# Kernel optimization log

Measured on AMD Instinct MI355X. Metric: run time of the kernel, lower is better.

Reference implementation:

```python
import jax, jax.numpy as jnp
import numpy as np

T, R, HEADS, H, L = 4, 8, 4, 128, 2
DK = H // HEADS
NPT = 25000
N = T * NPT
E = 600000
IN_DIMS = [512, 256, 128, 64]


def setup_inputs() -> dict:
    key = jax.random.key(0)
    ks = iter(jax.random.split(key, 64))
    d = {}
    # per-type raw node features (concatenation order = type order)
    for i, di in enumerate(IN_DIMS):
        d[f"nf{i}"] = jax.random.normal(next(ks), (NPT, di), jnp.float32)
    # per-type input encoder MLPs: Linear(di,256) -> ReLU -> Linear(256,H)
    for i, di in enumerate(IN_DIMS):
        d[f"enc_w1_{i}"] = jax.random.normal(next(ks), (di, 256), jnp.float32) * (1.0 / np.sqrt(di))
        d[f"enc_b1_{i}"] = jnp.zeros((256,), jnp.float32)
        d[f"enc_w2_{i}"] = jax.random.normal(next(ks), (256, H), jnp.float32) * (1.0 / np.sqrt(256))
        d[f"enc_b2_{i}"] = jnp.zeros((H,), jnp.float32)
    # HGT conv params, stacked over L layers
    sc = 1.0 / np.sqrt(H)
    for nm in ["Wk", "Wq", "Wv", "Wa"]:
        d[nm] = jax.random.normal(next(ks), (L, T, H, H), jnp.float32) * sc
        d["b" + nm[1]] = jnp.zeros((L, T, H), jnp.float32)
    eye = jnp.broadcast_to(jnp.eye(DK, dtype=jnp.float32), (L, R, HEADS, DK, DK))
    d["rel_att"] = eye + 0.05 * jax.random.normal(next(ks), (L, R, HEADS, DK, DK), jnp.float32)
    d["rel_msg"] = eye + 0.05 * jax.random.normal(next(ks), (L, R, HEADS, DK, DK), jnp.float32)
    d["rel_pri"] = jnp.ones((L, R, HEADS), jnp.float32)
    d["skip"] = jnp.zeros((L, T), jnp.float32)  # sigmoid(0)=0.5 gate
    d["gamma"] = jnp.ones((L, H), jnp.float32)
    d["beta"] = jnp.zeros((L, H), jnp.float32)
    # graph structure
    d["node_types"] = jnp.repeat(jnp.arange(T, dtype=jnp.int32), NPT)
    d["edge_index"] = jax.random.randint(next(ks), (2, E), 0, N, jnp.int32)
    d["edge_types"] = jax.random.randint(next(ks), (E,), 0, R, jnp.int32)
    return d


def typed_linear(x, nt, W, b):
    # W: [T,H,H], b: [T,H]; select per-node-type transform
    allt = jnp.einsum('nd,tdh->tnh', x, W) + b[:, None, :]  # [T,N,H]
    return allt[nt, jnp.arange(x.shape[0])]  # [N,H]


def layer_norm(x, g, b):
    m = x.mean(-1, keepdims=True)
    v = jnp.var(x, -1, keepdims=True)
    return (x - m) * jax.lax.rsqrt(v + 1e-5) * g + b


def hgt_layer(h, nt, src, dst, et, Wk, bk, Wq, bq, Wv, bv, Wa, ba, ra, rm, rp, skip, g, be):
    n = h.shape[0]
    k = typed_linear(h, nt, Wk, bk).reshape(n, HEADS, DK)
    q = typed_linear(h, nt, Wq, bq).reshape(n, HEADS, DK)
    v = typed_linear(h, nt, Wv, bv).reshape(n, HEADS, DK)
    k_s, v_s, q_d = k[src], v[src], q[dst]  # [E,HEADS,DK]
    # relation-conditioned key/message transforms (small fixed loop over R relations)
    kt = jnp.zeros_like(k_s)
    mt = jnp.zeros_like(v_s)
    for r in range(R):
        msk = (et == r)[:, None, None]
        kt = kt + jnp.where(msk, jnp.einsum('ehd,hdf->ehf', k_s, ra[r]), 0.0)
        mt = mt + jnp.where(msk, jnp.einsum('ehd,hdf->ehf', v_s, rm[r]), 0.0)
    att = (q_d * kt).sum(-1) * rp[et] * (1.0 / np.sqrt(DK))  # [E,HEADS]
    # segment softmax over incoming edges of each target node
    amax = jax.ops.segment_max(att, dst, num_segments=n)
    amax = jnp.where(jnp.isfinite(amax), amax, 0.0)
    ea = jnp.exp(att - amax[dst])
    den = jax.ops.segment_sum(ea, dst, num_segments=n)
    w = ea / jnp.maximum(den[dst], 1e-9)
    res = jax.ops.segment_sum(w[:, :, None] * mt, dst, num_segments=n).reshape(n, H)
    trans = typed_linear(jax.nn.gelu(res, approximate=False), nt, Wa, ba)
    alpha = jax.nn.sigmoid(skip)[nt][:, None]
    out = trans * alpha + h * (1.0 - alpha)
    return layer_norm(out, g, be)


def reference(nf0, nf1, nf2, nf3,
              enc_w1_0, enc_b1_0, enc_w2_0, enc_b2_0,
              enc_w1_1, enc_b1_1, enc_w2_1, enc_b2_1,
              enc_w1_2, enc_b1_2, enc_w2_2, enc_b2_2,
              enc_w1_3, enc_b1_3, enc_w2_3, enc_b2_3,
              Wk, bk, Wq, bq, Wv, bv, Wa, ba,
              rel_att, rel_msg, rel_pri, skip, gamma, beta,
              node_types, edge_index, edge_types):
    encs = [(enc_w1_0, enc_b1_0, enc_w2_0, enc_b2_0),
            (enc_w1_1, enc_b1_1, enc_w2_1, enc_b2_1),
            (enc_w1_2, enc_b1_2, enc_w2_2, enc_b2_2),
            (enc_w1_3, enc_b1_3, enc_w2_3, enc_b2_3)]
    embs = [jax.nn.relu(nf @ w1 + b1) @ w2 + b2
            for nf, (w1, b1, w2, b2) in zip([nf0, nf1, nf2, nf3], encs)]
    h = jnp.concatenate(embs, axis=0)  # [N,H]; dropout is identity in eval mode
    src, dst = edge_index[0], edge_index[1]
    for l in range(L):
        h = hgt_layer(h, node_types, src, dst, edge_types,
                      Wk[l], bk[l], Wq[l], bq[l], Wv[l], bv[l], Wa[l], ba[l],
                      rel_att[l], rel_msg[l], rel_pri[l], skip[l], gamma[l], beta[l])
    return h
```

## Files before the change

kernel.cpp:

```cpp
#include <hip/hip_runtime.h>
#include <math.h>


#define NPT   25000
#define NN    100000
#define EE    600000
#define HD    128
#define NRELS 8

typedef unsigned short u16;
typedef unsigned int   u32;
using s16x8 = __attribute__((ext_vector_type(8))) short;
using f32x4 = __attribute__((ext_vector_type(4))) float;

__device__ __forceinline__ u16 f2bf(float x){
  u32 u = __float_as_uint(x);
  u += 0x7fffu + ((u >> 16) & 1u);
  return (u16)(u >> 16);
}
__device__ __forceinline__ float bf2f(u16 v){ return __uint_as_float(((u32)v) << 16); }

__global__ __launch_bounds__(256) void cast_tr(const float* __restrict__ in,
                                               u16* __restrict__ out, int K, int N){
  long b = blockIdx.y;
  const float* ib = in + b * (long)K * N;
  u16* ob = out + b * (long)K * N;
  int idx = blockIdx.x * 256 + threadIdx.x;
  if (idx < K * N){
    int n = idx / K, k = idx - n * K;
    ob[idx] = f2bf(ib[(long)k * N + n]);
  }
}

__global__ __launch_bounds__(256) void pack_rel(const float* __restrict__ ra,
                                                const float* __restrict__ rm,
                                                u16* __restrict__ out){
  int idx = blockIdx.x * 256 + threadIdx.x;
  if (idx >= 131072) return;
  int j = idx & 7, lane = (idx >> 3) & 63, nc = (idx >> 9) & 1;
  int h = (idx >> 10) & 3, r = (idx >> 12) & 7, mat = (idx >> 15) & 1, l = idx >> 16;
  const float* src = mat ? rm : ra;
  float v = src[(((long)l * 8 + r) * 4 + h) * 1024 + ((lane >> 4) * 8 + j) * 32 + nc * 16 + (lane & 15)];
  out[idx] = f2bf(v);
}

__global__ __launch_bounds__(256) void hist_key(const int* __restrict__ ei,
                                                const int* __restrict__ et,
                                                int* __restrict__ hist){
  int e = blockIdx.x * 256 + threadIdx.x;
  if (e < EE) atomicAdd(&hist[et[e] * NN + ei[EE + e]], 1);
}

__global__ __launch_bounds__(256) void scan_part_g(const int* __restrict__ in,
                                                   int* __restrict__ bsum, int n){
  __shared__ int sh[256];
  int i = blockIdx.x * 256 + threadIdx.x;
  sh[threadIdx.x] = (i < n) ? in[i] : 0;
  __syncthreads();
  for (int s = 128; s > 0; s >>= 1){
    if (threadIdx.x < s) sh[threadIdx.x] += sh[threadIdx.x + s];
    __syncthreads();
  }
  if (threadIdx.x == 0) bsum[blockIdx.x] = sh[0];
}

__global__ __launch_bounds__(512) void scan_bsum(int* bsum, int nb){
  __shared__ int sh[512];
  int t = threadIdx.x;
  int orig = (t < nb) ? bsum[t] : 0;
  sh[t] = orig;
  __syncthreads();
  for (int off = 1; off < 512; off <<= 1){
    int u = (t >= off) ? sh[t - off] : 0;
    __syncthreads();
    sh[t] += u;
    __syncthreads();
  }
  if (t < nb) bsum[t] = sh[t] - orig;
}

__global__ __launch_bounds__(256) void scan_fin_g(const int* __restrict__ in,
                                                  const int* __restrict__ bsum,
                                                  int* __restrict__ out, int n){
  __shared__ int sh[256];
  int i = blockIdx.x * 256 + threadIdx.x;
  int v = (i < n) ? in[i] : 0;
  sh[threadIdx.x] = v;
  __syncthreads();
  for (int off = 1; off < 256; off <<= 1){
    int u = (threadIdx.x >= off) ? sh[threadIdx.x - off] : 0;
    __syncthreads();
    sh[threadIdx.x] += u;
    __syncthreads();
  }
  if (i < n) out[i] = sh[threadIdx.x] - v + bsum[blockIdx.x];
}

__global__ void extract_offs(const int* __restrict__ cur, int* __restrict__ meta){
  int r = threadIdx.x;
  if (r < NRELS) meta[16 + r] = cur[r * NN];
  if (r == 0) meta[24] = EE;
}

__global__ __launch_bounds__(256) void scatter_key(const int* __restrict__ ei,
                                                   const int* __restrict__ et,
                                                   int* __restrict__ cur,
                                                   int* __restrict__ ss, int* __restrict__ sd){
  int e = blockIdx.x * 256 + threadIdx.x;
  if (e < EE){
    int s = ei[e], d = ei[EE + e];
    int p = atomicAdd(&cur[et[e] * NN + d], 1);
    ss[p] = s;
    sd[p] = d;
  }
}

__global__ __launch_bounds__(256) void hist_dst(const int* __restrict__ sd, int* __restrict__ hist){
  int e = blockIdx.x * 256 + threadIdx.x;
  if (e < EE) atomicAdd(&hist[sd[e]], 1);
}

__global__ __launch_bounds__(256) void scan_fin(const int* __restrict__ hist,
                                                const int* __restrict__ bsum,
                                                int* __restrict__ rowp, int* __restrict__ cursor){
  __shared__ int sh[256];
  int i = blockIdx.x * 256 + threadIdx.x;
  int v = (i < NN) ? hist[i] : 0;
  sh[threadIdx.x] = v;
  __syncthreads();
  for (int off = 1; off < 256; off <<= 1){
    int u = (threadIdx.x >= off) ? sh[threadIdx.x - off] : 0;
    __syncthreads();
    sh[threadIdx.x] += u;
    __syncthreads();
  }
  int excl = sh[threadIdx.x] - v + bsum[blockIdx.x];
  if (i < NN){ rowp[i] = excl; cursor[i] = excl; }
  if (i == NN - 1) rowp[NN] = excl + v;
}

__global__ __launch_bounds__(256) void dp_scat(const int* __restrict__ sd,
                                               int* __restrict__ cursor, int* __restrict__ dp){
  int e = blockIdx.x * 256 + threadIdx.x;
  if (e < EE) dp[e] = atomicAdd(&cursor[sd[e]], 1);
}

template<bool A_F32, bool RELU, bool OUTF32, bool OUTBF16>
__global__ __launch_bounds__(256)
void gemm_k(const void* __restrict__ Ap, const u16* __restrict__ Bt,
            const float* __restrict__ bias,
            float* __restrict__ Cf, u16* __restrict__ Cbf,
            int M, int N, int K, int sAr, int sB, int sBias, int sCr,
            int ldC, int colOff)
{
  __shared__ __align__(16) u16 As[128 * 40];
  __shared__ __align__(16) u16 Bs[128 * 40];
  int z = blockIdx.z;
  int tid = threadIdx.x, wv = tid >> 6, lane = tid & 63;
  int m0 = blockIdx.x * 128, n0 = blockIdx.y * 128;
  int wm = (wv >> 1) * 64, wn = (wv & 1) * 64;
  long aBase = (long)z * sAr * K;
  const u16*   Ab  = (const u16*)Ap;
  const float* Afp = (const float*)Ap;
  const u16* Bz = Bt + (long)z * sB;
  const float* biz = bias + (long)z * sBias;
  long cRow0 = (long)z * sCr;
  int r2 = tid >> 1, hf = tid & 1;

  f32x4 acc[4][4];
  #pragma unroll
  for (int i = 0; i < 4; i++)
    #pragma unroll
    for (int j = 0; j < 4; j++) acc[i][j] = (f32x4){0.f, 0.f, 0.f, 0.f};

  for (int kk = 0; kk < K; kk += 32){
    {
      int gm = m0 + r2;
      #pragma unroll
      for (int c = 0; c < 2; c++){
        int ko = kk + c * 16 + hf * 8;
        union { u16 us[8]; uint4 v; } pk;
        if (gm < M){
          if (!A_F32){
            pk.v = *(const uint4*)(Ab + aBase + (long)gm * K + ko);
          } else {
            const float* s = Afp + aBase + (long)gm * K + ko;
            float4 f0 = *(const float4*)s;
            float4 f1 = *(const float4*)(s + 4);
            pk.us[0] = f2bf(f0.x); pk.us[1] = f2bf(f0.y); pk.us[2] = f2bf(f0.z); pk.us[3] = f2bf(f0.w);
            pk.us[4] = f2bf(f1.x); pk.us[5] = f2bf(f1.y); pk.us[6] = f2bf(f1.z); pk.us[7] = f2bf(f1.w);
          }
        } else {
          pk.v = make_uint4(0u, 0u, 0u, 0u);
        }
        *(uint4*)&As[r2 * 40 + c * 16 + hf * 8] = pk.v;
      }
    }
    {
      int gn = n0 + r2;
      #pragma unroll
      for (int c = 0; c < 2; c++){
        int ko = kk + c * 16 + hf * 8;
        uint4 v;
        if (gn < N) v = *(const uint4*)(Bz + (long)gn * K + ko);
        else        v = make_uint4(0u, 0u, 0u, 0u);
        *(uint4*)&Bs[r2 * 40 + c * 16 + hf * 8] = v;
      }
    }
    __syncthreads();
    s16x8 af[4], bfr[4];
    int rr = lane & 15, q8 = (lane >> 4) * 8;
    #pragma unroll
    for (int mt = 0; mt < 4; mt++) af[mt]  = *(const s16x8*)&As[(wm + mt * 16 + rr) * 40 + q8];
    #pragma unroll
    for (int nt = 0; nt < 4; nt++) bfr[nt] = *(const s16x8*)&Bs[(wn + nt * 16 + rr) * 40 + q8];
    #pragma unroll
    for (int mt = 0; mt < 4; mt++)
      #pragma unroll
      for (int nt = 0; nt < 4; nt++)
        acc[mt][nt] = __builtin_amdgcn_mfma_f32_16x16x32_bf16(af[mt], bfr[nt], acc[mt][nt], 0, 0, 0);
    __syncthreads();
  }
  int col = lane & 15, row4 = (lane >> 4) * 4;
  #pragma unroll
  for (int mt = 0; mt < 4; mt++){
    #pragma unroll
    for (int nt = 0; nt < 4; nt++){
      int gn = n0 + wn + nt * 16 + col;
      float bb = (gn < N) ? biz[gn] : 0.f;
      #pragma unroll
      for (int r = 0; r < 4; r++){
        int gm = m0 + wm + mt * 16 + row4 + r;
        if (gm < M && gn < N){
          float vv = acc[mt][nt][r] + bb;
          if (RELU) vv = fmaxf(vv, 0.f);
          long ci = (cRow0 + gm) * (long)ldC + colOff + gn;
          if (OUTF32)  Cf[ci]  = vv;
          if (OUTBF16) Cbf[ci] = f2bf(vv);
        }
      }
    }
  }
}

__global__ __launch_bounds__(256)
void edge_fused(const u16* __restrict__ kvb, const u16* __restrict__ qb,
                const int* __restrict__ ss, const int* __restrict__ sd,
                const int* __restrict__ dp, const int* __restrict__ offs,
                const u16* __restrict__ relpk, const float* __restrict__ rp,
                float* __restrict__ att, u16* __restrict__ wt, int l)
{
  __shared__ __align__(16) u16 ktS[4][16][136];
  int r = blockIdx.y;
  int lo = offs[r], hi = offs[r + 1];
  int base = lo + blockIdx.x * 64;
  if (base >= hi) return;
  int cnt = hi - base; if (cnt > 64) cnt = 64;
  int tid = threadIdx.x, wv = tid >> 6, lane = tid & 63;
  if (wv * 16 >= cnt) return;
  int wcnt = cnt - wv * 16; if (wcnt > 16) wcnt = 16;
  int m = lane & 15, g = lane >> 4;
  int ebase = base + wv * 16;

  int mq = lane >> 2, part = lane & 3;
  int mqc = (mq < wcnt) ? mq : (wcnt - 1);
  int dnq = sd[ebase + mqc];
  int dpq = dp[ebase + mqc];
  const u16* qrow = qb + (long)dnq * 128 + part * 32;
  uint4 qv[4];
  #pragma unroll
  for (int j = 0; j < 4; j++) qv[j] = *(const uint4*)(qrow + j * 8);

  int mm = (m < wcnt) ? m : (wcnt - 1);
  int s_ = ss[ebase + mm];
  const u16* krow = kvb + (long)s_ * 256;
  s16x8 ak[4], av[4];
  #pragma unroll
  for (int h = 0; h < 4; h++){
    ak[h] = *(const s16x8*)(krow + h * 32 + g * 8);
    av[h] = *(const s16x8*)(krow + 128 + h * 32 + g * 8);
  }

  const u16* relA = relpk + (((long)l * 2) * 8 + r) * 4096;
  f32x4 tt[4][2];
  #pragma unroll
  for (int h = 0; h < 4; h++)
    #pragma unroll
    for (int nc = 0; nc < 2; nc++){
      s16x8 b = *(const s16x8*)(relA + h * 1024 + nc * 512 + lane * 8);
      tt[h][nc] = __builtin_amdgcn_mfma_f32_16x16x32_bf16(ak[h], b, (f32x4){0.f,0.f,0.f,0.f}, 0, 0, 0);
    }
  int col = lane & 15, row4 = (lane >> 4) * 4;
  #pragma unroll
  for (int h = 0; h < 4; h++)
    #pragma unroll
    for (int nc = 0; nc < 2; nc++)
      #pragma unroll
      for (int rr = 0; rr < 4; rr++)
        ktS[wv][row4 + rr][h * 32 + nc * 16 + col] = f2bf(tt[h][nc][rr]);
  __asm__ volatile("s_waitcnt lgkmcnt(0)" ::: "memory");

  {
    const u16* ktrow = &ktS[wv][mq][part * 32];
    float p = 0.f;
    #pragma unroll
    for (int j = 0; j < 4; j++){
      uint4 kk4 = *(const uint4*)(ktrow + j * 8);
      uint4 qq4 = qv[j];
      const u32* kw = (const u32*)&kk4;
      const u32* qw = (const u32*)&qq4;
      #pragma unroll
      for (int t = 0; t < 4; t++){
        u32 kk = kw[t], qq = qw[t];
        p = fmaf(bf2f((u16)(kk & 0xffffu)), bf2f((u16)(qq & 0xffffu)), p);
        p = fmaf(__uint_as_float(kk & 0xffff0000u), __uint_as_float(qq & 0xffff0000u), p);
      }
    }
    if (mq < wcnt)
      att[(long)dpq * 4 + part] = p * rp[r * 4 + part] * 0.17677669529663689f;
  }
  __asm__ volatile("s_waitcnt lgkmcnt(0)" ::: "memory");

  const u16* relM = relpk + (((long)l * 2 + 1) * 8 + r) * 4096;
  #pragma unroll
  for (int h = 0; h < 4; h++)
    #pragma unroll
    for (int nc = 0; nc < 2; nc++){
      s16x8 b = *(const s16x8*)(relM + h * 1024 + nc * 512 + lane * 8);
      tt[h][nc] = __builtin_amdgcn_mfma_f32_16x16x32_bf16(av[h], b, (f32x4){0.f,0.f,0.f,0.f}, 0, 0, 0);
    }
  #pragma unroll
  for (int h = 0; h < 4; h++)
    #pragma unroll
    for (int nc = 0; nc < 2; nc++)
      #pragma unroll
      for (int rr = 0; rr < 4; rr++)
        ktS[wv][row4 + rr][h * 32 + nc * 16 + col] = f2bf(tt[h][nc][rr]);
  __asm__ volatile("s_waitcnt lgkmcnt(0)" ::: "memory");

  if (mq < wcnt){
    #pragma unroll
    for (int j = 0; j < 4; j++){
      uint4 v = *(const uint4*)&ktS[wv][mq][part * 32 + j * 8];
      *(uint4*)(wt + (long)dpq * 128 + part * 32 + j * 8) = v;
    }
  }
}

__global__ __launch_bounds__(256)
void seg_reduce(const float* __restrict__ att, const u16* __restrict__ wt,
                const int* __restrict__ rowp, u16* __restrict__ gA)
{
  __shared__ __align__(16) float eas[4][64][4];
  int wv = threadIdx.x >> 6, lane = threadIdx.x & 63;
  int d = blockIdx.x * 4 + wv;
  if (d >= NN) return;
  int first = rowp[d], last = rowp[d + 1];
  int hsel = lane >> 4;
  float m0 = -1e30f, m1 = -1e30f, m2 = -1e30f, m3 = -1e30f;
  float den0 = 0, den1 = 0, den2 = 0, den3 = 0;
  float acc0 = 0, acc1 = 0;
  for (int c0 = first; c0 < last; c0 += 64){
    int cnt = min(64, last - c0);
    float4 a;
    if (lane < cnt) a = *(const float4*)(att + (long)(c0 + lane) * 4);
    else            a = make_float4(-1e30f, -1e30f, -1e30f, -1e30f);
    float c_0 = a.x, c_1 = a.y, c_2 = a.z, c_3 = a.w;
    #pragma unroll
    for (int mm = 1; mm < 64; mm <<= 1){
      c_0 = fmaxf(c_0, __shfl_xor(c_0, mm));
      c_1 = fmaxf(c_1, __shfl_xor(c_1, mm));
      c_2 = fmaxf(c_2, __shfl_xor(c_2, mm));
      c_3 = fmaxf(c_3, __shfl_xor(c_3, mm));
    }
    float n0 = fmaxf(m0, c_0), n1 = fmaxf(m1, c_1), n2 = fmaxf(m2, c_2), n3 = fmaxf(m3, c_3);
    float r0 = __expf(m0 - n0), r1 = __expf(m1 - n1), r2 = __expf(m2 - n2), r3 = __expf(m3 - n3);
    den0 *= r0; den1 *= r1; den2 *= r2; den3 *= r3;
    float rsel = (hsel == 0) ? r0 : (hsel == 1) ? r1 : (hsel == 2) ? r2 : r3;
    acc0 *= rsel; acc1 *= rsel;
    m0 = n0; m1 = n1; m2 = n2; m3 = n3;
    float e_0 = 0, e_1 = 0, e_2 = 0, e_3 = 0;
    if (lane < cnt){
      e_0 = __expf(a.x - m0); e_1 = __expf(a.y - m1);
      e_2 = __expf(a.z - m2); e_3 = __expf(a.w - m3);
    }
    float s0 = e_0, s1 = e_1, s2 = e_2, s3 = e_3;
    #pragma unroll
    for (int mm = 1; mm < 64; mm <<= 1){
      s0 += __shfl_xor(s0, mm); s1 += __shfl_xor(s1, mm);
      s2 += __shfl_xor(s2, mm); s3 += __shfl_xor(s3, mm);
    }
    den0 += s0; den1 += s1; den2 += s2; den3 += s3;
    *(float4*)&eas[wv][lane][0] = make_float4(e_0, e_1, e_2, e_3);
    for (int i = 0; i < cnt; i++){
      float ea = eas[wv][i][hsel];
      u32 w = *(const u32*)(wt + (long)(c0 + i) * HD + 2 * lane);
      acc0 = fmaf(ea, bf2f((u16)(w & 0xffffu)), acc0);
      acc1 = fmaf(ea, __uint_as_float(w & 0xffff0000u), acc1);
    }
  }
  float dh = (hsel == 0) ? den0 : (hsel == 1) ? den1 : (hsel == 2) ? den2 : den3;
  float x0 = acc0 / fmaxf(dh, 1e-9f);
  float x1 = acc1 / fmaxf(dh, 1e-9f);
  x0 = 0.5f * x0 * (1.0f + erff(x0 * 0.70710678118654752f));
  x1 = 0.5f * x1 * (1.0f + erff(x1 * 0.70710678118654752f));
  u32 o = (u32)f2bf(x0) | ((u32)f2bf(x1) << 16);
  *(u32*)(gA + (long)d * HD + 2 * lane) = o;
}

__global__ __launch_bounds__(256)
void combine_ln(const float* __restrict__ trans, float* __restrict__ h,
                u16* __restrict__ hb, const float* __restrict__ skl,
                const float* __restrict__ gm, const float* __restrict__ bt)
{
  int wv = threadIdx.x >> 6, lane = threadIdx.x & 63;
  int node = blockIdx.x * 4 + wv;
  if (node >= NN) return;
  int t = node / NPT;
  float alpha = 1.f / (1.f + __expf(-skl[t]));
  long b0 = (long)node * HD;
  float x0 = trans[b0 + lane]      * alpha + h[b0 + lane]      * (1.f - alpha);
  float x1 = trans[b0 + 64 + lane] * alpha + h[b0 + 64 + lane] * (1.f - alpha);
  float s = x0 + x1;
  #pragma unroll
  for (int m = 1; m < 64; m <<= 1) s += __shfl_xor(s, m);
  float mean = s * (1.f / HD);
  float d0 = x0 - mean, d1 = x1 - mean;
  float vs = d0 * d0 + d1 * d1;
  #pragma unroll
  for (int m = 1; m < 64; m <<= 1) vs += __shfl_xor(vs, m);
  float rstd = rsqrtf(vs * (1.f / HD) + 1e-5f);
  float y0 = d0 * rstd * gm[lane]      + bt[lane];
  float y1 = d1 * rstd * gm[64 + lane] + bt[64 + lane];
  h[b0 + lane] = y0;        h[b0 + 64 + lane] = y1;
  hb[b0 + lane] = f2bf(y0); hb[b0 + 64 + lane] = f2bf(y1);
}

extern "C" void kernel_launch(void* const* d_in, const int* in_sizes, int n_in,
                              void* d_out, int out_size, void* d_ws, size_t ws_size,
                              hipStream_t stream)
{
  const float* nf[4]  = {(const float*)d_in[0], (const float*)d_in[1], (const float*)d_in[2], (const float*)d_in[3]};
  const float* ew1[4] = {(const float*)d_in[4], (const float*)d_in[8],  (const float*)d_in[12], (const float*)d_in[16]};
  const float* eb1[4] = {(const float*)d_in[5], (const float*)d_in[9],  (const float*)d_in[13], (const float*)d_in[17]};
  const float* ew2[4] = {(const float*)d_in[6], (const float*)d_in[10], (const float*)d_in[14], (const float*)d_in[18]};
  const float* eb2[4] = {(const float*)d_in[7], (const float*)d_in[11], (const float*)d_in[15], (const float*)d_in[19]};
  const float* Wk = (const float*)d_in[20]; const float* bk = (const float*)d_in[21];
  const float* Wq = (const float*)d_in[22]; const float* bq = (const float*)d_in[23];
  const float* Wv = (const float*)d_in[24]; const float* bv = (const float*)d_in[25];
  const float* Wa = (const float*)d_in[26]; const float* ba = (const float*)d_in[27];
  const float* rel_att = (const float*)d_in[28];
  const float* rel_msg = (const float*)d_in[29];
  const float* rel_pri = (const float*)d_in[30];
  const float* skp = (const float*)d_in[31];
  const float* gma = (const float*)d_in[32];
  const float* bta = (const float*)d_in[33];
  const int* edge_index = (const int*)d_in[35];
  const int* edge_types = (const int*)d_in[36];
  float* out = (float*)d_out;
  char* ws = (char*)d_ws;

  u16*   kvb   = (u16*)  (ws + 0L);
  float* trans = (float*)(ws + 0L);
  u16*   qb    = (u16*)  (ws + 51200000L);
  u16*   gA    = (u16*)  (ws + 51200000L);
  u16*   wt    = (u16*)  (ws + 76800000L);
  u16*   hbf   = (u16*)  (ws + 76800000L);
  u16*   hid   = (u16*)  (ws + 102400000L);
  float* attb  = (float*)(ws + 230400000L);
  int*   hist800 = (int*)(ws + 230400000L);
  int*   cur800  = (int*)(ws + 233600128L);
  int*   b1      = (int*)(ws + 236800256L);
  int*   b2      = (int*)(ws + 236816384L);
  int*   bsum    = (int*)(ws + 236816512L);
  int*   ss    = (int*)  (ws + 240000000L);
  int*   sd    = (int*)  (ws + 242400000L);
  int*   dp    = (int*)  (ws + 244800000L);
  int*   rowp  = (int*)  (ws + 247200000L);
  int*   curs  = (int*)  (ws + 247600128L);
  u16*   relpk = (u16*)  (ws + 247600128L);
  int*   meta  = (int*)  (ws + 248000128L);
  u16*   w1t   = (u16*)  (ws + 248000384L);
  u16*   w2t   = (u16*)  (ws + 248491904L);
  u16*   wkt   = (u16*)  (ws + 248754048L);
  u16*   wqt   = (u16*)  (ws + 249016192L);
  u16*   wvt   = (u16*)  (ws + 249278336L);
  u16*   wat   = (u16*)  (ws + 249540480L);

  int  di[4]  = {512, 256, 128, 64};
  long w1o[4] = {0, 131072, 196608, 229376};

  for (int i = 0; i < 4; i++){
    cast_tr<<<dim3(di[i], 1), 256, 0, stream>>>(ew1[i], w1t + w1o[i], di[i], 256);
    cast_tr<<<dim3(128, 1),  256, 0, stream>>>(ew2[i], w2t + (long)i * 32768, 256, 128);
  }
  cast_tr<<<dim3(64, 8), 256, 0, stream>>>(Wk, wkt, 128, 128);
  cast_tr<<<dim3(64, 8), 256, 0, stream>>>(Wq, wqt, 128, 128);
  cast_tr<<<dim3(64, 8), 256, 0, stream>>>(Wv, wvt, 128, 128);
  cast_tr<<<dim3(64, 8), 256, 0, stream>>>(Wa, wat, 128, 128);

  hipMemsetAsync(hist800, 0, 3200000, stream);
  hist_key   <<<2344, 256, 0, stream>>>(edge_index, edge_types, hist800);
  scan_part_g<<<3125, 256, 0, stream>>>(hist800, b1, 800000);
  scan_part_g<<<13,   256, 0, stream>>>(b1, b2, 3125);
  scan_bsum  <<<1,    512, 0, stream>>>(b2, 13);
  scan_fin_g <<<13,   256, 0, stream>>>(b1, b2, b1, 3125);
  scan_fin_g <<<3125, 256, 0, stream>>>(hist800, b1, cur800, 800000);
  extract_offs<<<1, 64, 0, stream>>>(cur800, meta);
  scatter_key<<<2344, 256, 0, stream>>>(edge_index, edge_types, cur800, ss, sd);

  hipMemsetAsync(curs, 0, 400000, stream);
  hist_dst   <<<2344, 256, 0, stream>>>(sd, curs);
  scan_part_g<<<391, 256, 0, stream>>>(curs, bsum, NN);
  scan_bsum  <<<1, 512, 0, stream>>>(bsum, 391);
  scan_fin   <<<391, 256, 0, stream>>>(curs, bsum, rowp, curs);
  dp_scat    <<<2344, 256, 0, stream>>>(sd, curs, dp);

  pack_rel<<<512, 256, 0, stream>>>(rel_att, rel_msg, relpk);

  for (int i = 0; i < 4; i++){
    gemm_k<true,  true,  false, true><<<dim3(196, 2, 1), 256, 0, stream>>>(
        nf[i], w1t + w1o[i], eb1[i], nullptr, hid, NPT, 256, di[i], 0, 0, 0, 0, 256, 0);
    gemm_k<false, false, true,  true><<<dim3(196, 1, 1), 256, 0, stream>>>(
        hid, w2t + (long)i * 32768, eb2[i],
        out + (long)i * NPT * HD, hbf + (long)i * NPT * HD, NPT, 128, 256, 0, 0, 0, 0, 128, 0);
  }

  for (int l = 0; l < 2; l++){
    gemm_k<false, false, false, true><<<dim3(196, 1, 4), 256, 0, stream>>>(
        hbf, wkt + (long)l * 65536, bk + l * 512, nullptr, kvb,
        NPT, 128, 128, NPT, 16384, 128, NPT, 256, 0);
    gemm_k<false, false, false, true><<<dim3(196, 1, 4), 256, 0, stream>>>(
        hbf, wvt + (long)l * 65536, bv + l * 512, nullptr, kvb,
        NPT, 128, 128, NPT, 16384, 128, NPT, 256, 128);
    gemm_k<false, false, false, true><<<dim3(196, 1, 4), 256, 0, stream>>>(
        hbf, wqt + (long)l * 65536, bq + l * 512, nullptr, qb,
        NPT, 128, 128, NPT, 16384, 128, NPT, 128, 0);

    edge_fused<<<dim3(1200, 8), 256, 0, stream>>>(
        kvb, qb, ss, sd, dp, meta + 16, relpk, rel_pri + l * 32, attb, wt, l);

    seg_reduce<<<25000, 256, 0, stream>>>(attb, wt, rowp, gA);

    gemm_k<false, false, true, false><<<dim3(196, 1, 4), 256, 0, stream>>>(
        gA, wat + (long)l * 65536, ba + l * 512, trans, nullptr,
        NPT, 128, 128, NPT, 16384, 128, NPT, 128, 0);

    combine_ln<<<25000, 256, 0, stream>>>(
        trans, out, hbf, skp + l * 4, gma + l * 128, bta + l * 128);
  }
}
```

Baseline: 1.191 ms.

## Fuse K/V/Q GEMMs, fuse output GEMM with skip+LayerNorm, batch weight casts

Merges the twelve weight cast/transpose launches into a single multi-segment kernel. Replaces the three separate K, V and Q projection GEMMs with one launch whose blocks pick the weight set by block index. Fuses the output projection GEMM with the skip gate and LayerNorm, using a cross-wave shared-memory reduction, so the fp32 trans buffer is never written or read. This cuts launch count and global memory traffic, but LayerNorm now uses the E[x^2]-mean^2 variance form, which loses some precision.

Measured after the change: 1.111 ms. 6.7% less time.

```diff
diff --git a/kernel.cpp b/kernel.cpp
--- a/kernel.cpp
+++ b/kernel.cpp
@@ -20,16 +20,26 @@
 }
 __device__ __forceinline__ float bf2f(u16 v){ return __uint_as_float(((u32)v) << 16); }
 
-__global__ __launch_bounds__(256) void cast_tr(const float* __restrict__ in,
-                                               u16* __restrict__ out, int K, int N){
-  long b = blockIdx.y;
-  const float* ib = in + b * (long)K * N;
-  u16* ob = out + b * (long)K * N;
-  int idx = blockIdx.x * 256 + threadIdx.x;
-  if (idx < K * N){
-    int n = idx / K, k = idx - n * K;
-    ob[idx] = f2bf(ib[(long)k * N + n]);
-  }
+struct CastArgs {
+  const float* src[12];
+  u16* dst[12];
+  int K[12], N[12], B[12];
+  int blk0[13];
+};
+
+__global__ __launch_bounds__(256) void cast_all(CastArgs a){
+  int blk = blockIdx.x;
+  int s = 0;
+  while (s < 11 && blk >= a.blk0[s + 1]) s++;
+  long idx = (long)(blk - a.blk0[s]) * 256 + threadIdx.x;
+  int K = a.K[s], N = a.N[s];
+  long per = (long)K * N;
+  long tot = per * a.B[s];
+  if (idx >= tot) return;
+  int b = (int)(idx / per);
+  long rem = idx - (long)b * per;
+  int n = (int)(rem / K), k = (int)(rem - (long)n * K);
+  a.dst[s][idx] = f2bf(a.src[s][(long)b * per + (long)k * N + n]);
 }
 
 __global__ __launch_bounds__(256) void pack_rel(const float* __restrict__ ra,
@@ -244,6 +254,217 @@
 }
 
 __global__ __launch_bounds__(256)
+void gemm_kvq(const u16* __restrict__ A,
+              const u16* __restrict__ BK, const u16* __restrict__ BV, const u16* __restrict__ BQ,
+              const float* __restrict__ bK, const float* __restrict__ bV, const float* __restrict__ bQ,
+              u16* __restrict__ kvb, u16* __restrict__ qb)
+{
+  __shared__ __align__(16) u16 As[128 * 40];
+  __shared__ __align__(16) u16 Bs[128 * 40];
+  int bx = blockIdx.x;
+  int grp = bx % 3;
+  int m0 = (bx / 3) * 128;
+  int z = blockIdx.z;
+  int tid = threadIdx.x, wv = tid >> 6, lane = tid & 63;
+  int wm = (wv >> 1) * 64, wn = (wv & 1) * 64;
+  long aBase = (long)z * NPT * 128;
+  const u16* Bz = ((grp == 0) ? BK : (grp == 1) ? BV : BQ) + (long)z * 16384;
+  const float* biz = ((grp == 0) ? bK : (grp == 1) ? bV : bQ) + z * 128;
+  u16* C = (grp == 2) ? qb : kvb;
+  int ldC = (grp == 2) ? 128 : 256;
+  int colOff = (grp == 1) ? 128 : 0;
+  long cRow0 = (long)z * NPT;
+  int r2 = tid >> 1, hf = tid & 1;
+
+  f32x4 acc[4][4];
+  #pragma unroll
+  for (int i = 0; i < 4; i++)
+    #pragma unroll
+    for (int j = 0; j < 4; j++) acc[i][j] = (f32x4){0.f, 0.f, 0.f, 0.f};
+
+  for (int kk = 0; kk < 128; kk += 32){
+    {
+      int gm = m0 + r2;
+      #pragma unroll
+      for (int c = 0; c < 2; c++){
+        int ko = kk + c * 16 + hf * 8;
+        uint4 v;
+        if (gm < NPT) v = *(const uint4*)(A + aBase + (long)gm * 128 + ko);
+        else          v = make_uint4(0u, 0u, 0u, 0u);
+        *(uint4*)&As[r2 * 40 + c * 16 + hf * 8] = v;
+      }
+    }
+    {
+      int gn = r2;
+      #pragma unroll
+      for (int c = 0; c < 2; c++){
+        int ko = kk + c * 16 + hf * 8;
+        uint4 v = *(const uint4*)(Bz + (long)gn * 128 + ko);
+        *(uint4*)&Bs[r2 * 40 + c * 16 + hf * 8] = v;
+      }
+    }
+    __syncthreads();
+    s16x8 af[4], bfr[4];
+    int rr = lane & 15, q8 = (lane >> 4) * 8;
+    #pragma unroll
+    for (int mt = 0; mt < 4; mt++) af[mt]  = *(const s16x8*)&As[(wm + mt * 16 + rr) * 40 + q8];
+    #pragma unroll
+    for (int nt = 0; nt < 4; nt++) bfr[nt] = *(const s16x8*)&Bs[(wn + nt * 16 + rr) * 40 + q8];
+    #pragma unroll
+    for (int mt = 0; mt < 4; mt++)
+      #pragma unroll
+      for (int nt = 0; nt < 4; nt++)
+        acc[mt][nt] = __builtin_amdgcn_mfma_f32_16x16x32_bf16(af[mt], bfr[nt], acc[mt][nt], 0, 0, 0);
+    __syncthreads();
+  }
+  int col = lane & 15, row4 = (lane >> 4) * 4;
+  #pragma unroll
+  for (int mt = 0; mt < 4; mt++){
+    #pragma unroll
+    for (int nt = 0; nt < 4; nt++){
+      int gn = wn + nt * 16 + col;
+      float bb = biz[gn];
+      #pragma unroll
+      for (int r = 0; r < 4; r++){
+        int gm = m0 + wm + mt * 16 + row4 + r;
+        if (gm < NPT){
+          float vv = acc[mt][nt][r] + bb;
+          C[(cRow0 + gm) * (long)ldC + colOff + gn] = f2bf(vv);
+        }
+      }
+    }
+  }
+}
+
+__global__ __launch_bounds__(256)
+void gemm_ln(const u16* __restrict__ A, const u16* __restrict__ Bt,
+             const float* __restrict__ bias,
+             float* __restrict__ h, u16* __restrict__ hb,
+             const float* __restrict__ skl, const float* __restrict__ gmv,
+             const float* __restrict__ btv)
+{
+  __shared__ __align__(16) u16 As[128 * 40];
+  __shared__ __align__(16) u16 Bs[128 * 40];
+  __shared__ float red[128][4];
+  int z = blockIdx.z;
+  int tid = threadIdx.x, wv = tid >> 6, lane = tid & 63;
+  int m0 = blockIdx.x * 128;
+  int wm = (wv >> 1) * 64, wn = (wv & 1) * 64;
+  long aBase = (long)z * NPT * 128;
+  const u16* Bz = Bt + (long)z * 16384;
+  const float* biz = bias + z * 128;
+  int r2 = tid >> 1, hf = tid & 1;
+
+  f32x4 acc[4][4];
+  #pragma unroll
+  for (int i = 0; i < 4; i++)
+    #pragma unroll
+    for (int j = 0; j < 4; j++) acc[i][j] = (f32x4){0.f, 0.f, 0.f, 0.f};
+
+  for (int kk = 0; kk < 128; kk += 32){
+    {
+      int gm = m0 + r2;
+      #pragma unroll
+      for (int c = 0; c < 2; c++){
+        int ko = kk + c * 16 + hf * 8;
+        uint4 v;
+        if (gm < NPT) v = *(const uint4*)(A + aBase + (long)gm * 128 + ko);
+        else          v = make_uint4(0u, 0u, 0u, 0u);
+        *(uint4*)&As[r2 * 40 + c * 16 + hf * 8] = v;
+      }
+    }
+    {
+      int gn = r2;
+      #pragma unroll
+      for (int c = 0; c < 2; c++){
+        int ko = kk + c * 16 + hf * 8;
+        uint4 v = *(const uint4*)(Bz + (long)gn * 128 + ko);
+        *(uint4*)&Bs[r2 * 40 + c * 16 + hf * 8] = v;
+      }
+    }
+    __syncthreads();
+    s16x8 af[4], bfr[4];
+    int rr = lane & 15, q8 = (lane >> 4) * 8;
+    #pragma unroll
+    for (int mt = 0; mt < 4; mt++) af[mt]  = *(const s16x8*)&As[(wm + mt * 16 + rr) * 40 + q8];
+    #pragma unroll
+    for (int nt = 0; nt < 4; nt++) bfr[nt] = *(const s16x8*)&Bs[(wn + nt * 16 + rr) * 40 + q8];
+    #pragma unroll
+    for (int mt = 0; mt < 4; mt++)
+      #pragma unroll
+      for (int nt = 0; nt < 4; nt++)
+        acc[mt][nt] = __builtin_amdgcn_mfma_f32_16x16x32_bf16(af[mt], bfr[nt], acc[mt][nt], 0, 0, 0);
+    __syncthreads();
+  }
+
+  int col = lane & 15, q = lane >> 4, row4 = q * 4;
+  float alpha = 1.f / (1.f + __expf(-skl[z]));
+  float bb[4], ga[4], be[4];
+  #pragma unroll
+  for (int nt = 0; nt < 4; nt++){
+    int gn = wn + nt * 16 + col;
+    bb[nt] = biz[gn];
+    ga[nt] = gmv[gn];
+    be[nt] = btv[gn];
+  }
+
+  #pragma unroll
+  for (int mt = 0; mt < 4; mt++){
+    #pragma unroll
+    for (int rr = 0; rr < 4; rr++){
+      int gmr = m0 + wm + mt * 16 + row4 + rr;
+      bool ok = gmr < NPT;
+      long rb = ((long)z * NPT + gmr) * HD;
+      float p1 = 0.f, p2 = 0.f;
+      #pragma unroll
+      for (int nt = 0; nt < 4; nt++){
+        int gn = wn + nt * 16 + col;
+        float hv = ok ? h[rb + gn] : 0.f;
+        float vf = (acc[mt][nt][rr] + bb[nt]) * alpha + hv * (1.f - alpha);
+        acc[mt][nt][rr] = vf;
+        p1 += vf;
+        p2 += vf * vf;
+      }
+      #pragma unroll
+      for (int mk = 1; mk < 16; mk <<= 1){
+        p1 += __shfl_xor(p1, mk);
+        p2 += __shfl_xor(p2, mk);
+      }
+      if (col == 0){
+        int lr = wm + mt * 16 + row4 + rr;
+        red[lr][2 * (wn >> 6)]     = p1;
+        red[lr][2 * (wn >> 6) + 1] = p2;
+      }
+    }
+  }
+  __syncthreads();
+
+  #pragma unroll
+  for (int mt = 0; mt < 4; mt++){
+    #pragma unroll
+    for (int rr = 0; rr < 4; rr++){
+      int lr = wm + mt * 16 + row4 + rr;
+      int gmr = m0 + lr;
+      float ts1 = red[lr][0] + red[lr][2];
+      float ts2 = red[lr][1] + red[lr][3];
+      float mean = ts1 * (1.f / HD);
+      float var = ts2 * (1.f / HD) - mean * mean;
+      float rstd = rsqrtf(fmaxf(var, 0.f) + 1e-5f);
+      if (gmr < NPT){
+        long rb = ((long)z * NPT + gmr) * HD;
+        #pragma unroll
+        for (int nt = 0; nt < 4; nt++){
+          int gn = wn + nt * 16 + col;
+          float y = (acc[mt][nt][rr] - mean) * rstd * ga[nt] + be[nt];
+          h[rb + gn]  = y;
+          hb[rb + gn] = f2bf(y);
+        }
+      }
+    }
+  }
+}
+
+__global__ __launch_bounds__(256)
 void edge_fused(const u16* __restrict__ kvb, const u16* __restrict__ qb,
                 const int* __restrict__ ss, const int* __restrict__ sd,
                 const int* __restrict__ dp, const int* __restrict__ offs,
@@ -406,34 +627,6 @@
   x1 = 0.5f * x1 * (1.0f + erff(x1 * 0.70710678118654752f));
   u32 o = (u32)f2bf(x0) | ((u32)f2bf(x1) << 16);
   *(u32*)(gA + (long)d * HD + 2 * lane) = o;
-}
-
-__global__ __launch_bounds__(256)
-void combine_ln(const float* __restrict__ trans, float* __restrict__ h,
-                u16* __restrict__ hb, const float* __restrict__ skl,
-                const float* __restrict__ gm, const float* __restrict__ bt)
-{
-  int wv = threadIdx.x >> 6, lane = threadIdx.x & 63;
-  int node = blockIdx.x * 4 + wv;
-  if (node >= NN) return;
-  int t = node / NPT;
-  float alpha = 1.f / (1.f + __expf(-skl[t]));
-  long b0 = (long)node * HD;
-  float x0 = trans[b0 + lane]      * alpha + h[b0 + lane]      * (1.f - alpha);
-  float x1 = trans[b0 + 64 + lane] * alpha + h[b0 + 64 + lane] * (1.f - alpha);
-  float s = x0 + x1;
-  #pragma unroll
-  for (int m = 1; m < 64; m <<= 1) s += __shfl_xor(s, m);
-  float mean = s * (1.f / HD);
-  float d0 = x0 - mean, d1 = x1 - mean;
-  float vs = d0 * d0 + d1 * d1;
-  #pragma unroll
-  for (int m = 1; m < 64; m <<= 1) vs += __shfl_xor(vs, m);
-  float rstd = rsqrtf(vs * (1.f / HD) + 1e-5f);
-  float y0 = d0 * rstd * gm[lane]      + bt[lane];
-  float y1 = d1 * rstd * gm[64 + lane] + bt[64 + lane];
-  h[b0 + lane] = y0;        h[b0 + 64 + lane] = y1;
-  hb[b0 + lane] = f2bf(y0); hb[b0 + 64 + lane] = f2bf(y1);
 }
 
 extern "C" void kernel_launch(void* const* d_in, const int* in_sizes, int n_in,
@@ -461,7 +654,6 @@
   char* ws = (char*)d_ws;
 
   u16*   kvb   = (u16*)  (ws + 0L);
-  float* trans = (float*)(ws + 0L);
   u16*   qb    = (u16*)  (ws + 51200000L);
   u16*   gA    = (u16*)  (ws + 51200000L);
   u16*   wt    = (u16*)  (ws + 76800000L);
@@ -490,14 +682,24 @@
   int  di[4]  = {512, 256, 128, 64};
   long w1o[4] = {0, 131072, 196608, 229376};
 
-  for (int i = 0; i < 4; i++){
-    cast_tr<<<dim3(di[i], 1), 256, 0, stream>>>(ew1[i], w1t + w1o[i], di[i], 256);
-    cast_tr<<<dim3(128, 1),  256, 0, stream>>>(ew2[i], w2t + (long)i * 32768, 256, 128);
-  }
-  cast_tr<<<dim3(64, 8), 256, 0, stream>>>(Wk, wkt, 128, 128);
-  cast_tr<<<dim3(64, 8), 256, 0, stream>>>(Wq, wqt, 128, 128);
-  cast_tr<<<dim3(64, 8), 256, 0, stream>>>(Wv, wvt, 128, 128);
-  cast_tr<<<dim3(64, 8), 256, 0, stream>>>(Wa, wat, 128, 128);
+  {
+    CastArgs ca;
+    for (int i = 0; i < 4; i++){
+      ca.src[i] = ew1[i]; ca.dst[i] = w1t + w1o[i]; ca.K[i] = di[i]; ca.N[i] = 256; ca.B[i] = 1;
+      ca.src[4 + i] = ew2[i]; ca.dst[4 + i] = w2t + (long)i * 32768; ca.K[4 + i] = 256; ca.N[4 + i] = 128; ca.B[4 + i] = 1;
+    }
+    const float* bigs[4] = {Wk, Wq, Wv, Wa};
+    u16* bigd[4] = {wkt, wqt, wvt, wat};
+    for (int i = 0; i < 4; i++){
+      ca.src[8 + i] = bigs[i]; ca.dst[8 + i] = bigd[i];
+      ca.K[8 + i] = 128; ca.N[8 + i] = 128; ca.B[8 + i] = 8;
+    }
+    int blocks[12] = {512, 256, 128, 64, 128, 128, 128, 128, 512, 512, 512, 512};
+    int acc = 0;
+    for (int i = 0; i < 12; i++){ ca.blk0[i] = acc; acc += blocks[i]; }
+    ca.blk0[12] = acc;
+    cast_all<<<acc, 256, 0, stream>>>(ca);
+  }
 
   hipMemsetAsync(hist800, 0, 3200000, stream);
   hist_key   <<<2344, 256, 0, stream>>>(edge_index, edge_types, hist800);
@@ -527,26 +729,17 @@
   }
 
   for (int l = 0; l < 2; l++){
-    gemm_k<false, false, false, true><<<dim3(196, 1, 4), 256, 0, stream>>>(
-        hbf, wkt + (long)l * 65536, bk + l * 512, nullptr, kvb,
-        NPT, 128, 128, NPT, 16384, 128, NPT, 256, 0);
-    gemm_k<false, false, false, true><<<dim3(196, 1, 4), 256, 0, stream>>>(
-        hbf, wvt + (long)l * 65536, bv + l * 512, nullptr, kvb,
-        NPT, 128, 128, NPT, 16384, 128, NPT, 256, 128);
-    gemm_k<false, false, false, true><<<dim3(196, 1, 4), 256, 0, stream>>>(
-        hbf, wqt + (long)l * 65536, bq + l * 512, nullptr, qb,
-        NPT, 128, 128, NPT, 16384, 128, NPT, 128, 0);
+    gemm_kvq<<<dim3(588, 1, 4), 256, 0, stream>>>(
+        hbf, wkt + (long)l * 65536, wvt + (long)l * 65536, wqt + (long)l * 65536,
+        bk + l * 512, bv + l * 512, bq + l * 512, kvb, qb);
 
     edge_fused<<<dim3(1200, 8), 256, 0, stream>>>(
         kvb, qb, ss, sd, dp, meta + 16, relpk, rel_pri + l * 32, attb, wt, l);
 
     seg_reduce<<<25000, 256, 0, stream>>>(attb, wt, rowp, gA);
 
-    gemm_k<false, false, true, false><<<dim3(196, 1, 4), 256, 0, stream>>>(
-        gA, wat + (long)l * 65536, ba + l * 512, trans, nullptr,
-        NPT, 128, 128, NPT, 16384, 128, NPT, 128, 0);
-
-    combine_ln<<<25000, 256, 0, stream>>>(
-        trans, out, hbf, skp + l * 4, gma + l * 128, bta + l * 128);
-  }
-}
+    gemm_ln<<<dim3(196, 1, 4), 256, 0, stream>>>(
+        gA, wat + (long)l * 65536, ba + l * 512, out, hbf,
+        skp + l * 4, gma + l * 128, bta + l * 128);
+  }
+}
```
